# Kernel optimization log

Hardware: AMD Instinct MI355X
Metric: run time of the kernel (lower is better)

Reference implementation:

```python
import jax, jax.numpy as jnp
import numpy as np

TEMP1, TEMP2, TEMP3 = 4.0, 5.0, 10.0  # forward() default temps
EPS = 1e-8


def setup_inputs() -> dict:
    key = jax.random.key(0)
    k1, k2 = jax.random.split(key)
    B, L, D = 64, 64, 512
    return {
        "ecg_embs": jax.random.normal(k1, (B, L, D), dtype=jnp.float32),
        "sent_embs": jax.random.normal(k2, (B, L, D), dtype=jnp.float32),
    }


def reference(ecg_embs, sent_embs):
    # Fully-batched version of the original per-sample Python loop.
    # i indexes the sentence (query) sample, j the ecg (context) sample.
    B, L, D = ecg_embs.shape
    # scores[i,j,s,q] = <ecg[j,s,:], sent[i,q,:]>  == contextT @ query in torch
    scores = jnp.einsum('jsd,iqd->ijsq', ecg_embs, sent_embs)
    # 1st softmax over query axis q
    attn = jax.nn.softmax(scores, axis=-1)
    # transpose to (i,j,q,s), temperature-scale, 2nd softmax over source axis s
    attn = jax.nn.softmax(TEMP1 * jnp.swapaxes(attn, -1, -2), axis=-1)  # (i,j,q,s)
    # weightedContext[i,j,q,:] = sum_s attn[i,j,q,s] * ecg[j,s,:]
    wctx = jnp.einsum('ijqs,jsd->ijqd', attn, ecg_embs)
    sent = sent_embs[:, None]  # (i,1,q,d) broadcast over j
    w12 = jnp.sum(sent * wctx, axis=-1)
    w1 = jnp.linalg.norm(sent, axis=-1)
    w2 = jnp.linalg.norm(wctx, axis=-1)
    cos = w12 / jnp.maximum(w1 * w2, EPS)  # (i,j,q)
    # row_sim.mul_(temp2).exp_().sum(dim=1).log() ; similarities[j,i] (cat along dim=1)
    sim = TEMP3 * jnp.log(jnp.sum(jnp.exp(TEMP2 * cos), axis=-1)).T  # (j,i)
    labels = jnp.arange(B)
    logp0 = jax.nn.log_softmax(sim, axis=-1)
    logp1 = jax.nn.log_softmax(sim.T, axis=-1)
    loss0 = -jnp.mean(logp0[labels, labels])
    loss1 = -jnp.mean(logp1[labels, labels])
    # att_maps: list of attn[i] from iteration i == diagonal (i==j) attention,
    # each shaped (1, queryL, ih=1, iw=sourceL); stacked -> (B, 1, L, 1, L)
    att_maps = attn[labels, labels][:, None, :, None, :]
    return (loss0 + loss1) / 2.0, att_maps
```

## Files before the change

kernel.cpp:

```cpp
#include <hip/hip_runtime.h>
#include <math.h>

typedef __attribute__((ext_vector_type(8))) short short8;
typedef __attribute__((ext_vector_type(4))) float f32x4;
typedef unsigned int uint;
typedef unsigned short ushort;

#define T1 4.0f
#define T2 5.0f
#define T3 10.0f
#define EPSF 1e-8f

__device__ inline ushort f2bf(float x) {
    union { float f; uint u; } a; a.f = x;
    uint r = a.u + 0x7FFFu + ((a.u >> 16) & 1u);
    return (ushort)(r >> 16);
}
__device__ inline float bf2f(ushort h) {
    union { uint u; float f; } a; a.u = ((uint)h) << 16;
    return a.f;
}

#define GLDS(gsrc, ldst) \
    __builtin_amdgcn_global_load_lds( \
        (const __attribute__((address_space(1))) uint*)(gsrc), \
        (__attribute__((address_space(3))) uint*)(ldst), 16, 0, 0)

__global__ __launch_bounds__(256) void prepg_kernel(
        const float* __restrict__ ecg, const float* __restrict__ sent,
        char* __restrict__ EH, char* __restrict__ EL,
        char* __restrict__ SH, char* __restrict__ SL,
        char* __restrict__ Gp, float* __restrict__ w1) {
    __shared__ __align__(16) char plds[8192];
    const int bid = blockIdx.x;
    const int tid = threadIdx.x;
    const int r = tid >> 2, cq = tid & 3;
    const int phys = (cq + (r >> 1)) & 3;

    if (bid < 64) {
        const int j = bid;
        const float* src = ecg + (size_t)j * 32768;
        char* dh = EH + (size_t)j * 65536;
        char* dl = EL + (size_t)j * 65536;
        const int wv = tid >> 6, lane = tid & 63;
        const int wq = wv >> 1, wn = wv & 1;
        const int quad = lane >> 4, ln = lane & 15;
        int ao[2], bo[2];
        #pragma unroll
        for (int mi = 0; mi < 2; mi++) {
            int R = 32 * wq + 16 * mi + ln;
            ao[mi] = R * 64 + ((quad + (R >> 1)) & 3) * 16;
        }
        #pragma unroll
        for (int ni = 0; ni < 2; ni++) {
            int R = 32 * wn + 16 * ni + ln;
            bo[ni] = R * 64 + ((quad + (R >> 1)) & 3) * 16;
        }
        f32x4 acc[2][2];
        #pragma unroll
        for (int a = 0; a < 2; a++)
            #pragma unroll
            for (int b = 0; b < 2; b++) acc[a][b] = (f32x4){0.f, 0.f, 0.f, 0.f};

        for (int kc = 0; kc < 16; kc++) {
            const float4* p = (const float4*)(src + (size_t)r * 512 + kc * 32 + cq * 8);
            float4 va = p[0], vb = p[1];
            ushort h0 = f2bf(va.x), h1 = f2bf(va.y), h2 = f2bf(va.z), h3 = f2bf(va.w);
            ushort h4 = f2bf(vb.x), h5 = f2bf(vb.y), h6 = f2bf(vb.z), h7 = f2bf(vb.w);
            uint4 H;
            H.x = (uint)h0 | ((uint)h1 << 16); H.y = (uint)h2 | ((uint)h3 << 16);
            H.z = (uint)h4 | ((uint)h5 << 16); H.w = (uint)h6 | ((uint)h7 << 16);
            uint4 L;
            L.x = (uint)f2bf(va.x - bf2f(h0)) | ((uint)f2bf(va.y - bf2f(h1)) << 16);
            L.y = (uint)f2bf(va.z - bf2f(h2)) | ((uint)f2bf(va.w - bf2f(h3)) << 16);
            L.z = (uint)f2bf(vb.x - bf2f(h4)) | ((uint)f2bf(vb.y - bf2f(h5)) << 16);
            L.w = (uint)f2bf(vb.z - bf2f(h6)) | ((uint)f2bf(vb.w - bf2f(h7)) << 16);
            __syncthreads();
            *(uint4*)(plds + r * 64 + phys * 16)        = H;
            *(uint4*)(plds + 4096 + r * 64 + phys * 16) = L;
            *(uint4*)(dh + (size_t)kc * 4096 + r * 64 + phys * 16) = H;
            *(uint4*)(dl + (size_t)kc * 4096 + r * 64 + phys * 16) = L;
            __syncthreads();
            short8 ah[2], al[2], bh[2], bl[2];
            #pragma unroll
            for (int mi = 0; mi < 2; mi++) {
                ah[mi] = *(const short8*)(plds + ao[mi]);
                al[mi] = *(const short8*)(plds + 4096 + ao[mi]);
            }
            #pragma unroll
            for (int ni = 0; ni < 2; ni++) {
                bh[ni] = *(const short8*)(plds + bo[ni]);
                bl[ni] = *(const short8*)(plds + 4096 + bo[ni]);
            }
            #pragma unroll
            for (int mi = 0; mi < 2; mi++)
                #pragma unroll
                for (int ni = 0; ni < 2; ni++) {
                    acc[mi][ni] = __builtin_amdgcn_mfma_f32_16x16x32_bf16(ah[mi], bh[ni], acc[mi][ni], 0, 0, 0);
                    acc[mi][ni] = __builtin_amdgcn_mfma_f32_16x16x32_bf16(ah[mi], bl[ni], acc[mi][ni], 0, 0, 0);
                    acc[mi][ni] = __builtin_amdgcn_mfma_f32_16x16x32_bf16(al[mi], bh[ni], acc[mi][ni], 0, 0, 0);
                }
        }
        #pragma unroll
        for (int mi = 0; mi < 2; mi++)
            #pragma unroll
            for (int ni = 0; ni < 2; ni++)
                #pragma unroll
                for (int rr = 0; rr < 4; rr++) {
                    int t = 32 * wq + 16 * mi + quad * 4 + rr;
                    int u = 32 * wn + 16 * ni + ln;
                    float g = acc[mi][ni][rr];
                    ushort h = f2bf(g);
                    ushort l = f2bf(g - bf2f(h));
                    char* base = Gp + (size_t)j * 16384 + t * 128 + (((u >> 3) + t) & 7) * 16 + (u & 7) * 2;
                    *(ushort*)base = h;
                    *(ushort*)(base + 8192) = l;
                }
    } else {
        const int idx = bid - 64;
        const float* src = sent + (size_t)idx * 32768;
        char* dh = SH + (size_t)idx * 65536;
        char* dl = SL + (size_t)idx * 65536;
        float s2 = 0.f;
        for (int kc = 0; kc < 16; kc++) {
            const float4* p = (const float4*)(src + (size_t)r * 512 + kc * 32 + cq * 8);
            float4 va = p[0], vb = p[1];
            s2 += va.x * va.x + va.y * va.y + va.z * va.z + va.w * va.w +
                  vb.x * vb.x + vb.y * vb.y + vb.z * vb.z + vb.w * vb.w;
            ushort h0 = f2bf(va.x), h1 = f2bf(va.y), h2 = f2bf(va.z), h3 = f2bf(va.w);
            ushort h4 = f2bf(vb.x), h5 = f2bf(vb.y), h6 = f2bf(vb.z), h7 = f2bf(vb.w);
            uint4 H;
            H.x = (uint)h0 | ((uint)h1 << 16); H.y = (uint)h2 | ((uint)h3 << 16);
            H.z = (uint)h4 | ((uint)h5 << 16); H.w = (uint)h6 | ((uint)h7 << 16);
            uint4 L;
            L.x = (uint)f2bf(va.x - bf2f(h0)) | ((uint)f2bf(va.y - bf2f(h1)) << 16);
            L.y = (uint)f2bf(va.z - bf2f(h2)) | ((uint)f2bf(va.w - bf2f(h3)) << 16);
            L.z = (uint)f2bf(vb.x - bf2f(h4)) | ((uint)f2bf(vb.y - bf2f(h5)) << 16);
            L.w = (uint)f2bf(vb.z - bf2f(h6)) | ((uint)f2bf(vb.w - bf2f(h7)) << 16);
            *(uint4*)(dh + (size_t)kc * 4096 + r * 64 + phys * 16) = H;
            *(uint4*)(dl + (size_t)kc * 4096 + r * 64 + phys * 16) = L;
        }
        ((float*)plds)[tid] = s2;
        __syncthreads();
        if (tid < 64) {
            const float* q = (const float*)plds + tid * 4;
            w1[idx * 64 + tid] = sqrtf(q[0] + q[1] + q[2] + q[3]);
        }
    }
}

__global__ __launch_bounds__(256, 4) void pair_kernel(
        const char* __restrict__ EH, const char* __restrict__ EL,
        const char* __restrict__ SH, const char* __restrict__ SL,
        const char* __restrict__ Gp, const float* __restrict__ w1g,
        float* __restrict__ simval, float* __restrict__ out) {

    __shared__ __align__(16) char lds[32768];
    __shared__ __align__(16) float mz[64];
    __shared__ float w12all[256], w2all[256];
    __shared__ float w2part[64 * 9];

    const int tid = threadIdx.x;
    const int bn = blockIdx.x;
    const int xcd = bn & 7, slot = bn >> 3;
    const int T = xcd * 8 + (slot >> 4);
    const int wp = slot & 15;
    const int bi = (T >> 3) * 4 + (wp >> 2);
    const int bj = (T & 7) * 4 + (wp & 3);
    const int i0 = bi * 2, j0 = bj * 2;

    const int wv = tid >> 6, lane = tid & 63;
    const int wq = wv >> 1, wn = wv & 1;
    const int quad = lane >> 4, ln = lane & 15;

    int aoff[4], boff[4];
    #pragma unroll
    for (int mi = 0; mi < 4; mi++) {
        int R = 64 * (mi >> 1) + 32 * wq + 16 * (mi & 1) + ln;
        aoff[mi] = R * 64 + ((quad + (R >> 1)) & 3) * 16;
    }
    #pragma unroll
    for (int ni = 0; ni < 4; ni++) {
        int R = 64 * (ni >> 1) + 32 * wn + 16 * (ni & 1) + ln;
        boff[ni] = 16384 + R * 64 + ((quad + (R >> 1)) & 3) * 16;
    }

    const char* gA; const char* gB; int ldoff;
    if (wv == 0)      { gA = EH + (size_t)j0 * 65536;       gB = EH + (size_t)(j0 + 1) * 65536; ldoff = 0; }
    else if (wv == 1) { gA = EL + (size_t)j0 * 65536;       gB = EL + (size_t)(j0 + 1) * 65536; ldoff = 8192; }
    else if (wv == 2) { gA = SH + (size_t)i0 * 65536;       gB = SH + (size_t)(i0 + 1) * 65536; ldoff = 16384; }
    else              { gA = SL + (size_t)i0 * 65536;       gB = SL + (size_t)(i0 + 1) * 65536; ldoff = 24576; }
    gA += lane * 16; gB += lane * 16;

    f32x4 acc[4][4];
    #pragma unroll
    for (int a = 0; a < 4; a++)
        #pragma unroll
        for (int b = 0; b < 4; b++) acc[a][b] = (f32x4){0.f, 0.f, 0.f, 0.f};

    for (int kc = 0; kc < 16; kc++) {
        #pragma unroll
        for (int n = 0; n < 4; n++) GLDS(gA + n * 1024, lds + ldoff + n * 1024);
        #pragma unroll
        for (int n = 0; n < 4; n++) GLDS(gB + n * 1024, lds + ldoff + 4096 + n * 1024);
        gA += 4096; gB += 4096;
        __syncthreads();
        short8 bh[4], bl[4];
        #pragma unroll
        for (int ni = 0; ni < 4; ni++) {
            bh[ni] = *(const short8*)(lds + boff[ni]);
            bl[ni] = *(const short8*)(lds + boff[ni] + 8192);
        }
        #pragma unroll
        for (int mi = 0; mi < 4; mi++) {
            short8 ah = *(const short8*)(lds + aoff[mi]);
            short8 al = *(const short8*)(lds + aoff[mi] + 8192);
            #pragma unroll
            for (int ni = 0; ni < 4; ni++) {
                acc[mi][ni] = __builtin_amdgcn_mfma_f32_16x16x32_bf16(ah, bh[ni], acc[mi][ni], 0, 0, 0);
                acc[mi][ni] = __builtin_amdgcn_mfma_f32_16x16x32_bf16(ah, bl[ni], acc[mi][ni], 0, 0, 0);
                acc[mi][ni] = __builtin_amdgcn_mfma_f32_16x16x32_bf16(al, bh[ni], acc[mi][ni], 0, 0, 0);
            }
        }
        __syncthreads();
    }

    char* Phi = lds + 16384;

    #pragma unroll
    for (int pr = 0; pr < 4; pr++) {
        const int a = pr >> 1, b = pr & 1;
        const int i = i0 + b, j = j0 + a;
        const char* Gpj = Gp + (size_t)j * 16384;

        #pragma unroll
        for (int dm = 0; dm < 2; dm++)
            #pragma unroll
            for (int dn = 0; dn < 2; dn++) {
                int s0 = 32 * wq + 16 * dm + quad * 4;
                int q  = 32 * wn + 16 * dn + ln;
                *(f32x4*)(lds + q * 256 + (((s0 >> 2) + q) & 15) * 16) = acc[2 * a + dm][2 * b + dn];
            }
        __syncthreads();

        {
            const int s = tid >> 2, c = tid & 3;
            float vv[16]; float m = -1e30f;
            #pragma unroll
            for (int t = 0; t < 16; t++) {
                int q = 16 * c + t;
                vv[t] = *(const float*)(lds + q * 256 + ((((s >> 2) + q) & 15) << 4) + ((s & 3) << 2));
                m = fmaxf(m, vv[t]);
            }
            m = fmaxf(m, __shfl_xor(m, 1));
            m = fmaxf(m, __shfl_xor(m, 2));
            float sum = 0.f;
            #pragma unroll
            for (int t = 0; t < 16; t++) sum += __expf(vv[t] - m);
            sum += __shfl_xor(sum, 1);
            sum += __shfl_xor(sum, 2);
            if (c == 0) mz[s] = m + __logf(sum);
        }
        __syncthreads();

        {
            const int q = tid >> 2, c = tid & 3;
            float sc[16], at[16], mzv[16];
            #pragma unroll
            for (int k = 0; k < 4; k++)
                *(f32x4*)(sc + 4 * k) = *(const f32x4*)(lds + q * 256 + (((4 * c + k) + q) & 15) * 16);
            #pragma unroll
            for (int k = 0; k < 4; k++)
                *(f32x4*)(mzv + 4 * k) = *(const f32x4*)(mz + 16 * c + 4 * k);
            float m2 = -1e30f;
            #pragma unroll
            for (int t = 0; t < 16; t++) {
                at[t] = __expf(sc[t] - mzv[t]);
                m2 = fmaxf(m2, T1 * at[t]);
            }
            m2 = fmaxf(m2, __shfl_xor(m2, 1));
            m2 = fmaxf(m2, __shfl_xor(m2, 2));
            float sum = 0.f;
            #pragma unroll
            for (int t = 0; t < 16; t++) { at[t] = __expf(T1 * at[t] - m2); sum += at[t]; }
            sum += __shfl_xor(sum, 1);
            sum += __shfl_xor(sum, 2);
            float inv = 1.f / sum;
            float p12 = 0.f;
            #pragma unroll
            for (int t = 0; t < 16; t++) { at[t] *= inv; p12 += at[t] * sc[t]; }
            p12 += __shfl_xor(p12, 1);
            p12 += __shfl_xor(p12, 2);
            if (c == 0) w12all[pr * 64 + q] = p12;

            if (i == j) {
                float* om = out + 1 + (size_t)i * 4096;
                #pragma unroll
                for (int t = 0; t < 16; t++) om[q * 64 + c * 16 + t] = at[t];
            }

            uint hw[8];
            #pragma unroll
            for (int e = 0; e < 8; e++)
                hw[e] = (uint)f2bf(at[2 * e]) | ((uint)f2bf(at[2 * e + 1]) << 16);
            int p0 = (2 * c + q) & 7, p1 = (2 * c + 1 + q) & 7;
            uint4 W;
            W.x = hw[0]; W.y = hw[1]; W.z = hw[2]; W.w = hw[3];
            *(uint4*)(Phi + q * 128 + p0 * 16) = W;
            W.x = hw[4]; W.y = hw[5]; W.z = hw[6]; W.w = hw[7];
            *(uint4*)(Phi + q * 128 + p1 * 16) = W;
        }
        __syncthreads();

        f32x4 acc2[2][2];
        #pragma unroll
        for (int x = 0; x < 2; x++)
            #pragma unroll
            for (int y = 0; y < 2; y++) acc2[x][y] = (f32x4){0.f, 0.f, 0.f, 0.f};
        #pragma unroll
        for (int ch = 0; ch < 2; ch++) {
            short8 pah[2], gbh[2], gbl[2];
            #pragma unroll
            for (int m2i = 0; m2i < 2; m2i++) {
                int q = 32 * wq + 16 * m2i + ln;
                pah[m2i] = *(const short8*)(Phi + q * 128 + (((ch * 4 + quad) + q) & 7) * 16);
            }
            #pragma unroll
            for (int n2i = 0; n2i < 2; n2i++) {
                int u = 32 * wn + 16 * n2i + ln;
                int ph = ((ch * 4 + quad) + u) & 7;
                gbh[n2i] = *(const short8*)(Gpj + u * 128 + ph * 16);
                gbl[n2i] = *(const short8*)(Gpj + 8192 + u * 128 + ph * 16);
            }
            #pragma unroll
            for (int m2i = 0; m2i < 2; m2i++)
                #pragma unroll
                for (int n2i = 0; n2i < 2; n2i++) {
                    acc2[m2i][n2i] = __builtin_amdgcn_mfma_f32_16x16x32_bf16(pah[m2i], gbh[n2i], acc2[m2i][n2i], 0, 0, 0);
                    acc2[m2i][n2i] = __builtin_amdgcn_mfma_f32_16x16x32_bf16(pah[m2i], gbl[n2i], acc2[m2i][n2i], 0, 0, 0);
                }
        }

        #pragma unroll
        for (int m2i = 0; m2i < 2; m2i++)
            #pragma unroll
            for (int rr = 0; rr < 4; rr++) {
                int q = 32 * wq + 16 * m2i + quad * 4 + rr;
                float p = 0.f;
                #pragma unroll
                for (int n2i = 0; n2i < 2; n2i++) {
                    int t = 32 * wn + 16 * n2i + ln;
                    float Pv = bf2f(*(const ushort*)(Phi + q * 128 +
                                     ((((t >> 3) + q) & 7) << 4) + ((t & 7) << 1)));
                    p += acc2[m2i][n2i][rr] * Pv;
                }
                p += __shfl_xor(p, 1);
                p += __shfl_xor(p, 2);
                if ((ln & 3) == 0) w2part[q * 9 + wn * 4 + (ln >> 2)] = p;
            }
        __syncthreads();

        if (tid < 64) {
            const float* wp9 = w2part + tid * 9;
            w2all[pr * 64 + tid] = wp9[0] + wp9[1] + wp9[2] + wp9[3] +
                                   wp9[4] + wp9[5] + wp9[6] + wp9[7];
        }
    }
    __syncthreads();

    {
        const int pr = wv;
        const int ii = i0 + (pr & 1), jj = j0 + (pr >> 1);
        float w2 = sqrtf(fmaxf(w2all[pr * 64 + lane], 0.f));
        float cosv = w12all[pr * 64 + lane] / fmaxf(w1g[ii * 64 + lane] * w2, EPSF);
        float e = __expf(T2 * cosv);
        #pragma unroll
        for (int off = 32; off; off >>= 1) e += __shfl_down(e, off);
        if (lane == 0) simval[ii * 64 + jj] = T3 * __logf(e);
    }
}

__global__ __launch_bounds__(256) void loss_kernel(const float* __restrict__ val,
                                                   float* __restrict__ out) {
    __shared__ float v[4096];
    const int tid = threadIdx.x;
    #pragma unroll
    for (int k = 0; k < 4; k++)
        ((float4*)v)[tid + k * 256] = ((const float4*)val)[tid + k * 256];
    __syncthreads();
    if (tid < 64) {
        int i = tid;
        float rmax = -1e30f, cmax = -1e30f;
        for (int jj = 0; jj < 64; jj++) {
            rmax = fmaxf(rmax, v[i * 64 + jj]);
            cmax = fmaxf(cmax, v[jj * 64 + i]);
        }
        float rs = 0.f, cs = 0.f;
        for (int jj = 0; jj < 64; jj++) {
            rs += __expf(v[i * 64 + jj] - rmax);
            cs += __expf(v[jj * 64 + i] - cmax);
        }
        float rlse = rmax + __logf(rs);
        float clse = cmax + __logf(cs);
        float part = 2.f * v[i * 64 + i] - rlse - clse;
        #pragma unroll
        for (int off = 32; off; off >>= 1) part += __shfl_down(part, off);
        if (i == 0) out[0] = -part / 128.f;
    }
}

extern "C" void kernel_launch(void* const* d_in, const int* in_sizes, int n_in,
                              void* d_out, int out_size, void* d_ws, size_t ws_size,
                              hipStream_t stream) {
    (void)in_sizes; (void)n_in; (void)out_size; (void)ws_size;
    const float* ecg  = (const float*)d_in[0];
    const float* sent = (const float*)d_in[1];
    float* out = (float*)d_out;

    char* ws = (char*)d_ws;
    float* w1v  = (float*)ws;
    float* simv = (float*)(ws + 16384);
    char* EH = ws + 32768;
    char* EL = EH + (size_t)64 * 65536;
    char* SH = EL + (size_t)64 * 65536;
    char* SL = SH + (size_t)64 * 65536;
    char* Gp = SL + (size_t)64 * 65536;

    prepg_kernel<<<128,  256, 0, stream>>>(ecg, sent, EH, EL, SH, SL, Gp, w1v);
    pair_kernel <<<1024, 256, 0, stream>>>(EH, EL, SH, SL, Gp, w1v, simv, out);
    loss_kernel <<<1,    256, 0, stream>>>(simv, out);
}
```

Baseline: 158.7 us.

## Batch two query samples per G-matrix pass and stage G in LDS

The per-pair loop is restructured so that for each context sample j, the attention matrices for both query samples i are computed first and stored as two bf16 P tiles. The G matrix for j is then loaded into LDS once with global_load_lds, and a single MFMA pass over 128 rows serves both pairs. This is meant to halve the reads of G, replace scattered global reads with LDS reads, and reduce the number of MFMA phases and barriers. In exchange it uses more LDS (a larger w2part), keeps more accumulators live, and moves the workspace offset.

```diff
diff --git a/kernel.cpp b/kernel.cpp
--- a/kernel.cpp
+++ b/kernel.cpp
@@ -158,7 +158,7 @@
     __shared__ __align__(16) char lds[32768];
     __shared__ __align__(16) float mz[64];
     __shared__ float w12all[256], w2all[256];
-    __shared__ float w2part[64 * 9];
+    __shared__ float w2part[128 * 9];
 
     const int tid = threadIdx.x;
     const int bn = blockIdx.x;
@@ -225,115 +225,127 @@
         __syncthreads();
     }
 
-    char* Phi = lds + 16384;
+    char* Pb = lds + 16384;
 
     #pragma unroll
-    for (int pr = 0; pr < 4; pr++) {
-        const int a = pr >> 1, b = pr & 1;
-        const int i = i0 + b, j = j0 + a;
-        const char* Gpj = Gp + (size_t)j * 16384;
-
-        #pragma unroll
-        for (int dm = 0; dm < 2; dm++)
-            #pragma unroll
-            for (int dn = 0; dn < 2; dn++) {
-                int s0 = 32 * wq + 16 * dm + quad * 4;
-                int q  = 32 * wn + 16 * dn + ln;
-                *(f32x4*)(lds + q * 256 + (((s0 >> 2) + q) & 15) * 16) = acc[2 * a + dm][2 * b + dn];
-            }
+    for (int a = 0; a < 2; a++) {
+        const int j = j0 + a;
+
+        #pragma unroll
+        for (int b = 0; b < 2; b++) {
+            const int i = i0 + b;
+            const int pr = 2 * a + b;
+
+            #pragma unroll
+            for (int dm = 0; dm < 2; dm++)
+                #pragma unroll
+                for (int dn = 0; dn < 2; dn++) {
+                    int s0 = 32 * wq + 16 * dm + quad * 4;
+                    int q  = 32 * wn + 16 * dn + ln;
+                    *(f32x4*)(lds + q * 256 + (((s0 >> 2) + q) & 15) * 16) = acc[2 * a + dm][2 * b + dn];
+                }
+            __syncthreads();
+
+            {
+                const int s = tid >> 2, c = tid & 3;
+                float vv[16]; float m = -1e30f;
+                #pragma unroll
+                for (int t = 0; t < 16; t++) {
+                    int q = 16 * c + t;
+                    vv[t] = *(const float*)(lds + q * 256 + ((((s >> 2) + q) & 15) << 4) + ((s & 3) << 2));
+                    m = fmaxf(m, vv[t]);
+                }
+                m = fmaxf(m, __shfl_xor(m, 1));
+                m = fmaxf(m, __shfl_xor(m, 2));
+                float sum = 0.f;
+                #pragma unroll
+                for (int t = 0; t < 16; t++) sum += __expf(vv[t] - m);
+                sum += __shfl_xor(sum, 1);
+                sum += __shfl_xor(sum, 2);
+                if (c == 0) mz[s] = m + __logf(sum);
+            }
+            __syncthreads();
+
+            {
+                const int q = tid >> 2, c = tid & 3;
+                float sc[16], at[16], mzv[16];
+                #pragma unroll
+                for (int k = 0; k < 4; k++)
+                    *(f32x4*)(sc + 4 * k) = *(const f32x4*)(lds + q * 256 + (((4 * c + k) + q) & 15) * 16);
+                #pragma unroll
+                for (int k = 0; k < 4; k++)
+                    *(f32x4*)(mzv + 4 * k) = *(const f32x4*)(mz + 16 * c + 4 * k);
+                float m2 = -1e30f;
+                #pragma unroll
+                for (int t = 0; t < 16; t++) {
+                    at[t] = __expf(sc[t] - mzv[t]);
+                    m2 = fmaxf(m2, T1 * at[t]);
+                }
+                m2 = fmaxf(m2, __shfl_xor(m2, 1));
+                m2 = fmaxf(m2, __shfl_xor(m2, 2));
+                float sum = 0.f;
+                #pragma unroll
+                for (int t = 0; t < 16; t++) { at[t] = __expf(T1 * at[t] - m2); sum += at[t]; }
+                sum += __shfl_xor(sum, 1);
+                sum += __shfl_xor(sum, 2);
+                float inv = 1.f / sum;
+                float p12 = 0.f;
+                #pragma unroll
+                for (int t = 0; t < 16; t++) { at[t] *= inv; p12 += at[t] * sc[t]; }
+                p12 += __shfl_xor(p12, 1);
+                p12 += __shfl_xor(p12, 2);
+                if (c == 0) w12all[pr * 64 + q] = p12;
+
+                if (i == j) {
+                    float* om = out + 1 + (size_t)i * 4096;
+                    #pragma unroll
+                    for (int t = 0; t < 16; t++) om[q * 64 + c * 16 + t] = at[t];
+                }
+
+                uint hw[8];
+                #pragma unroll
+                for (int e = 0; e < 8; e++)
+                    hw[e] = (uint)f2bf(at[2 * e]) | ((uint)f2bf(at[2 * e + 1]) << 16);
+                int p0 = (2 * c + q) & 7, p1 = (2 * c + 1 + q) & 7;
+                uint4 W;
+                W.x = hw[0]; W.y = hw[1]; W.z = hw[2]; W.w = hw[3];
+                *(uint4*)(Pb + b * 8192 + q * 128 + p0 * 16) = W;
+                W.x = hw[4]; W.y = hw[5]; W.z = hw[6]; W.w = hw[7];
+                *(uint4*)(Pb + b * 8192 + q * 128 + p1 * 16) = W;
+            }
+            __syncthreads();
+        }
+
+        {
+            const char* gs = Gp + (size_t)j * 16384 + wv * 4096 + lane * 16;
+            #pragma unroll
+            for (int k = 0; k < 4; k++)
+                GLDS(gs + k * 1024, lds + wv * 4096 + k * 1024);
+        }
         __syncthreads();
 
-        {
-            const int s = tid >> 2, c = tid & 3;
-            float vv[16]; float m = -1e30f;
-            #pragma unroll
-            for (int t = 0; t < 16; t++) {
-                int q = 16 * c + t;
-                vv[t] = *(const float*)(lds + q * 256 + ((((s >> 2) + q) & 15) << 4) + ((s & 3) << 2));
-                m = fmaxf(m, vv[t]);
-            }
-            m = fmaxf(m, __shfl_xor(m, 1));
-            m = fmaxf(m, __shfl_xor(m, 2));
-            float sum = 0.f;
-            #pragma unroll
-            for (int t = 0; t < 16; t++) sum += __expf(vv[t] - m);
-            sum += __shfl_xor(sum, 1);
-            sum += __shfl_xor(sum, 2);
-            if (c == 0) mz[s] = m + __logf(sum);
-        }
-        __syncthreads();
-
-        {
-            const int q = tid >> 2, c = tid & 3;
-            float sc[16], at[16], mzv[16];
-            #pragma unroll
-            for (int k = 0; k < 4; k++)
-                *(f32x4*)(sc + 4 * k) = *(const f32x4*)(lds + q * 256 + (((4 * c + k) + q) & 15) * 16);
-            #pragma unroll
-            for (int k = 0; k < 4; k++)
-                *(f32x4*)(mzv + 4 * k) = *(const f32x4*)(mz + 16 * c + 4 * k);
-            float m2 = -1e30f;
-            #pragma unroll
-            for (int t = 0; t < 16; t++) {
-                at[t] = __expf(sc[t] - mzv[t]);
-                m2 = fmaxf(m2, T1 * at[t]);
-            }
-            m2 = fmaxf(m2, __shfl_xor(m2, 1));
-            m2 = fmaxf(m2, __shfl_xor(m2, 2));
-            float sum = 0.f;
-            #pragma unroll
-            for (int t = 0; t < 16; t++) { at[t] = __expf(T1 * at[t] - m2); sum += at[t]; }
-            sum += __shfl_xor(sum, 1);
-            sum += __shfl_xor(sum, 2);
-            float inv = 1.f / sum;
-            float p12 = 0.f;
-            #pragma unroll
-            for (int t = 0; t < 16; t++) { at[t] *= inv; p12 += at[t] * sc[t]; }
-            p12 += __shfl_xor(p12, 1);
-            p12 += __shfl_xor(p12, 2);
-            if (c == 0) w12all[pr * 64 + q] = p12;
-
-            if (i == j) {
-                float* om = out + 1 + (size_t)i * 4096;
-                #pragma unroll
-                for (int t = 0; t < 16; t++) om[q * 64 + c * 16 + t] = at[t];
-            }
-
-            uint hw[8];
-            #pragma unroll
-            for (int e = 0; e < 8; e++)
-                hw[e] = (uint)f2bf(at[2 * e]) | ((uint)f2bf(at[2 * e + 1]) << 16);
-            int p0 = (2 * c + q) & 7, p1 = (2 * c + 1 + q) & 7;
-            uint4 W;
-            W.x = hw[0]; W.y = hw[1]; W.z = hw[2]; W.w = hw[3];
-            *(uint4*)(Phi + q * 128 + p0 * 16) = W;
-            W.x = hw[4]; W.y = hw[5]; W.z = hw[6]; W.w = hw[7];
-            *(uint4*)(Phi + q * 128 + p1 * 16) = W;
-        }
-        __syncthreads();
-
-        f32x4 acc2[2][2];
-        #pragma unroll
-        for (int x = 0; x < 2; x++)
+        f32x4 acc2[4][2];
+        #pragma unroll
+        for (int x = 0; x < 4; x++)
             #pragma unroll
             for (int y = 0; y < 2; y++) acc2[x][y] = (f32x4){0.f, 0.f, 0.f, 0.f};
         #pragma unroll
         for (int ch = 0; ch < 2; ch++) {
-            short8 pah[2], gbh[2], gbl[2];
-            #pragma unroll
-            for (int m2i = 0; m2i < 2; m2i++) {
-                int q = 32 * wq + 16 * m2i + ln;
-                pah[m2i] = *(const short8*)(Phi + q * 128 + (((ch * 4 + quad) + q) & 7) * 16);
+            short8 pah[4], gbh[2], gbl[2];
+            #pragma unroll
+            for (int m2i = 0; m2i < 4; m2i++) {
+                int rA = 64 * wq + 16 * m2i + ln;
+                pah[m2i] = *(const short8*)(Pb + rA * 128 + (((ch * 4 + quad) + rA) & 7) * 16);
             }
             #pragma unroll
             for (int n2i = 0; n2i < 2; n2i++) {
                 int u = 32 * wn + 16 * n2i + ln;
                 int ph = ((ch * 4 + quad) + u) & 7;
-                gbh[n2i] = *(const short8*)(Gpj + u * 128 + ph * 16);
-                gbl[n2i] = *(const short8*)(Gpj + 8192 + u * 128 + ph * 16);
-            }
-            #pragma unroll
-            for (int m2i = 0; m2i < 2; m2i++)
+                gbh[n2i] = *(const short8*)(lds + u * 128 + ph * 16);
+                gbl[n2i] = *(const short8*)(lds + 8192 + u * 128 + ph * 16);
+            }
+            #pragma unroll
+            for (int m2i = 0; m2i < 4; m2i++)
                 #pragma unroll
                 for (int n2i = 0; n2i < 2; n2i++) {
                     acc2[m2i][n2i] = __builtin_amdgcn_mfma_f32_16x16x32_bf16(pah[m2i], gbh[n2i], acc2[m2i][n2i], 0, 0, 0);
@@ -342,28 +354,28 @@
         }
 
         #pragma unroll
-        for (int m2i = 0; m2i < 2; m2i++)
+        for (int m2i = 0; m2i < 4; m2i++)
             #pragma unroll
             for (int rr = 0; rr < 4; rr++) {
-                int q = 32 * wq + 16 * m2i + quad * 4 + rr;
+                int rA = 64 * wq + 16 * m2i + quad * 4 + rr;
                 float p = 0.f;
                 #pragma unroll
                 for (int n2i = 0; n2i < 2; n2i++) {
                     int t = 32 * wn + 16 * n2i + ln;
-                    float Pv = bf2f(*(const ushort*)(Phi + q * 128 +
-                                     ((((t >> 3) + q) & 7) << 4) + ((t & 7) << 1)));
+                    float Pv = bf2f(*(const ushort*)(Pb + rA * 128 +
+                                     ((((t >> 3) + rA) & 7) << 4) + ((t & 7) << 1)));
                     p += acc2[m2i][n2i][rr] * Pv;
                 }
                 p += __shfl_xor(p, 1);
                 p += __shfl_xor(p, 2);
-                if ((ln & 3) == 0) w2part[q * 9 + wn * 4 + (ln >> 2)] = p;
+                if ((ln & 3) == 0) w2part[rA * 9 + wn * 4 + (ln >> 2)] = p;
             }
         __syncthreads();
 
-        if (tid < 64) {
+        if (tid < 128) {
             const float* wp9 = w2part + tid * 9;
-            w2all[pr * 64 + tid] = wp9[0] + wp9[1] + wp9[2] + wp9[3] +
-                                   wp9[4] + wp9[5] + wp9[6] + wp9[7];
+            w2all[(2 * a + (tid >> 6)) * 64 + (tid & 63)] =
+                wp9[0] + wp9[1] + wp9[2] + wp9[3] + wp9[4] + wp9[5] + wp9[6] + wp9[7];
         }
     }
     __syncthreads();
@@ -420,7 +432,7 @@
     char* ws = (char*)d_ws;
     float* w1v  = (float*)ws;
     float* simv = (float*)(ws + 16384);
-    char* EH = ws + 32768;
+    char* EH = ws + 65536;
     char* EL = EH + (size_t)64 * 65536;
     char* SH = EL + (size_t)64 * 65536;
     char* SL = SH + (size_t)64 * 65536;
```

Result: no change. 156.9 us (-1.2%).
